# Optimization experiments

Hardware: AMD Instinct MI355X
Metric: run time of the kernel (lower is better)

## Reference

```python
import jax, jax.numpy as jnp
import numpy as np

D_K = 64  # per-head dim, hardcoded in the original module


def setup_inputs() -> dict:
    key = jax.random.key(0)
    kq, kk, kv, km = jax.random.split(key, 4)
    B, H, S, D = 4, 16, 2048, 64
    Q = jax.random.normal(kq, (B, H, S, D), dtype=jnp.float32)
    K = jax.random.normal(kk, (B, H, S, D), dtype=jnp.float32)
    V = jax.random.normal(kv, (B, H, S, D), dtype=jnp.float32)
    attn_mask = jax.random.randint(km, (B, H, S, S), 0, 2).astype(jnp.bool_)
    return {"Q": Q, "K": K, "V": V, "attn_mask": attn_mask}


def reference(Q, K, V, attn_mask):
    # scores = Q @ K^T / sqrt(d_k)  -> [B, H, S, S]
    scale = 1.0 / np.sqrt(D_K).astype(np.float32)
    scores = jnp.einsum("bhqd,bhkd->bhqk", Q, K) * scale
    scores = jnp.where(attn_mask, jnp.float32(-1e9), scores)
    attn = jax.nn.softmax(scores, axis=-1)
    context = jnp.einsum("bhqk,bhkd->bhqd", attn, V)
    return (context, attn)
```

## Files before the change

### kernel.cpp

```cpp
#include <hip/hip_runtime.h>
#include <stdint.h>

#define S_LEN 2048
#define D_HEAD 64
#define NBH 64
#define QBLK 32
#define KBLK 64
#define NITER (S_LEN / KBLK)

typedef __attribute__((ext_vector_type(8))) short short8;
typedef __attribute__((ext_vector_type(4))) float f32x4;

#define KB_OFF   0
#define VT_OFF   24576
#define PRED_OFF 40960
#define P_OFF    49152
#define LP_OFF   53248
#define SMEM_BYTES 53504

#define FK_OFF  0
#define FVT_OFF 16384
#define FP_OFF  24576
#define FMB_OFF 28672
#define FLP_OFF 36864
#define FSMEM_BYTES 37120

__device__ __forceinline__ int swz1(int row, int b) {
  return row * 128 + (b ^ ((row & 7) << 4));
}
__device__ __forceinline__ int swz2(int row, int b) {
  return row * 128 + (b ^ (((row >> 1) & 7) << 4));
}

__device__ __forceinline__ short f2b(float x) {
  unsigned u = __float_as_uint(x);
  unsigned r = 0x7FFFu + ((u >> 16) & 1u);
  return (short)((u + r) >> 16);
}
__device__ __forceinline__ float b2f(short s) {
  return __uint_as_float(((unsigned)(unsigned short)s) << 16);
}

__device__ __forceinline__ void gload_lds16(const void* g, void* l) {
  __builtin_amdgcn_global_load_lds(
      (const __attribute__((address_space(1))) unsigned int*)g,
      (__attribute__((address_space(3))) unsigned int*)l, 16, 0, 0);
}

#define WAITBAR(N) do { \
  asm volatile("s_waitcnt vmcnt(" #N ") lgkmcnt(0)" ::: "memory"); \
  __builtin_amdgcn_s_barrier(); } while (0)

__global__ void detect_mask_kernel(const unsigned* m, int* flag) {
  unsigned v = m[blockIdx.x * 256 + threadIdx.x];
  if (v != 0u && v != 1u && v != 0x3F800000u) atomicOr(flag, 1);
}

__global__ void __launch_bounds__(256) convK_kernel(
    const float* __restrict__ in, short* __restrict__ out) {
  size_t i = ((size_t)blockIdx.x * 256 + threadIdx.x) * 8;
  float4 a = ((const float4*)(in + i))[0];
  float4 b = ((const float4*)(in + i))[1];
  short8 v;
  v[0] = f2b(a.x); v[1] = f2b(a.y); v[2] = f2b(a.z); v[3] = f2b(a.w);
  v[4] = f2b(b.x); v[5] = f2b(b.y); v[6] = f2b(b.z); v[7] = f2b(b.w);
  *(short8*)(out + i) = v;
}

__global__ void __launch_bounds__(256) convVT_kernel(
    const float* __restrict__ V, short* __restrict__ out) {
  __shared__ __align__(16) short t[64 * 72];
  int tid = threadIdx.x;
  int kb = blockIdx.x * 64, bh = blockIdx.y;
  const float* src = V + ((size_t)bh * S_LEN + kb) * D_HEAD;
#pragma unroll
  for (int j = 0; j < 4; ++j) {
    int key = j * 16 + (tid >> 4), d0 = (tid & 15) * 4;
    float4 f = *(const float4*)(src + (size_t)key * D_HEAD + d0);
    t[(d0 + 0) * 72 + key] = f2b(f.x);
    t[(d0 + 1) * 72 + key] = f2b(f.y);
    t[(d0 + 2) * 72 + key] = f2b(f.z);
    t[(d0 + 3) * 72 + key] = f2b(f.w);
  }
  __syncthreads();
  int row = tid >> 2, seg = tid & 3;
  short8 v0 = *(const short8*)(t + row * 72 + seg * 16);
  short8 v1 = *(const short8*)(t + row * 72 + seg * 16 + 8);
  short* dst = out + (size_t)bh * D_HEAD * S_LEN + (size_t)row * S_LEN + kb + seg * 16;
  *(short8*)dst = v0;
  *(short8*)(dst + 8) = v1;
}

template <bool BYTEMASK>
__device__ __forceinline__ void attn_fast(
    char* smem, const float* Qg, const void* maskg,
    const short* Kbf, const short* Vtb, float* ctxg, float* attng,
    int qb, int bh) {

  const int tid = threadIdx.x;
  const int w = tid >> 6, l = tid & 63;
  const int lg = l >> 4, li = l & 15;
  const int rh = w >> 1, ch = w & 1;
  const int qbase = qb * QBLK;
  const int row = tid >> 3, seg = tid & 7;

  const float* Qp = Qg + ((size_t)bh * S_LEN + qbase) * D_HEAD;
  const short* Kbp = Kbf + (size_t)bh * S_LEN * D_HEAD;
  const short* Vtp = Vtb + (size_t)bh * D_HEAD * S_LEN;
  float* attnp = attng + ((size_t)bh * S_LEN + qbase) * S_LEN;
  float* ctxp  = ctxg  + ((size_t)bh * S_LEN + qbase) * D_HEAD;
  const size_t mbase = ((size_t)bh * S_LEN + qbase + row) * S_LEN + seg * 8;

  auto stageK = [&](int it) {
    const int buf = it % 3;
    const int r0 = w * 16 + (l >> 3), ci = l & 7;
#pragma unroll
    for (int j = 0; j < 2; ++j) {
      int r = r0 + j * 8;
      const short* src = Kbp + ((size_t)(it * KBLK + r)) * D_HEAD + ((ci ^ (r & 7)) * 8);
      int off = __builtin_amdgcn_readfirstlane(buf * 8192 + (w * 16 + j * 8) * 128);
      gload_lds16(src, smem + KB_OFF + off);
    }
  };
  auto stageVt = [&](int it) {
    const int buf = it & 1;
    const int d0 = w * 16 + (l >> 3), ci = l & 7;
#pragma unroll
    for (int j = 0; j < 2; ++j) {
      int d = d0 + j * 8;
      const short* src = Vtp + (size_t)d * S_LEN + it * KBLK + ((ci ^ (d & 7)) * 8);
      int off = __builtin_amdgcn_readfirstlane(buf * 8192 + (w * 16 + j * 8) * 128);
      gload_lds16(src, smem + VT_OFF + off);
    }
  };

  auto qkt = [&](f32x4* accs, const short8* qf, int it) {
    char* kb = smem + KB_OFF + (it % 3) * 8192;
#pragma unroll
    for (int ct = 0; ct < 2; ++ct) {
      int key = ch * 32 + ct * 16 + li;
      short8 b0 = *(const short8*)(kb + swz1(key, lg * 16));
      short8 b1 = *(const short8*)(kb + swz1(key, 64 + lg * 16));
      accs[ct] = __builtin_amdgcn_mfma_f32_16x16x32_bf16(qf[0], b0, accs[ct], 0, 0, 0);
      accs[ct] = __builtin_amdgcn_mfma_f32_16x16x32_bf16(qf[1], b1, accs[ct], 0, 0, 0);
    }
  };

  struct MaskRegs { int4 a, b; uint2 c; };
  auto loadMask = [&](int it, MaskRegs& m) {
    if constexpr (BYTEMASK) {
      m.c = *(const uint2*)((const unsigned char*)maskg + mbase + it * KBLK);
    } else {
      const int* p = (const int*)maskg + mbase + it * KBLK;
      m.a = *(const int4*)p;
      m.b = *(const int4*)(p + 4);
    }
  };
  auto predWrite = [&](int it, const MaskRegs& m) {
    unsigned pb = 0;
    if constexpr (BYTEMASK) {
      unsigned lo = m.c.x, hi = m.c.y;
#pragma unroll
      for (int j = 0; j < 4; ++j) {
        pb |= (((lo >> (8 * j)) & 255u) != 0u ? 1u : 0u) << j;
        pb |= (((hi >> (8 * j)) & 255u) != 0u ? 1u : 0u) << (j + 4);
      }
    } else {
      pb |= (m.a.x != 0) ? 1u : 0u;
      pb |= (m.a.y != 0) ? 2u : 0u;
      pb |= (m.a.z != 0) ? 4u : 0u;
      pb |= (m.a.w != 0) ? 8u : 0u;
      pb |= (m.b.x != 0) ? 16u : 0u;
      pb |= (m.b.y != 0) ? 32u : 0u;
      pb |= (m.b.z != 0) ? 64u : 0u;
      pb |= (m.b.w != 0) ? 128u : 0u;
    }
    *(unsigned char*)(smem + PRED_OFF + it * 256 + row * 8 + seg) = (unsigned char)pb;
  };

  MaskRegs t0, t1, mA, mB;
  loadMask(0, t0); loadMask(1, t1); loadMask(2, mA); loadMask(3, mB);
  stageK(0); stageK(1);
  {
    const float* src = Qp + row * D_HEAD + seg * 8;
    float4 a = ((const float4*)src)[0];
    float4 b = ((const float4*)src)[1];
    short8 v;
    v[0] = f2b(a.x); v[1] = f2b(a.y); v[2] = f2b(a.z); v[3] = f2b(a.w);
    v[4] = f2b(b.x); v[5] = f2b(b.y); v[6] = f2b(b.z); v[7] = f2b(b.w);
    *(short8*)(smem + P_OFF + swz1(row, seg * 16)) = v;
  }
  __syncthreads();
  short8 qfrag[2];
  {
    int qr = rh * 16 + li;
    qfrag[0] = *(const short8*)(smem + P_OFF + swz1(qr, lg * 16));
    qfrag[1] = *(const short8*)(smem + P_OFF + swz1(qr, 64 + lg * 16));
  }
  predWrite(0, t0);
  predWrite(1, t1);

  float l_acc[4] = {0.f, 0.f, 0.f, 0.f};

  auto p1iter = [&](int i, MaskRegs& m) {
    f32x4 accs[2] = {{0.f,0.f,0.f,0.f},{0.f,0.f,0.f,0.f}};
    qkt(accs, qfrag, i);
    if (i <= 27) {
      if constexpr (BYTEMASK) WAITBAR(1); else WAITBAR(2);
    } else {
      WAITBAR(0);
    }
    if (i + 2 < NITER) stageK(i + 2);
    if (i + 2 < NITER) predWrite(i + 2, m);
    if (i + 4 < NITER) loadMask(i + 4, m);
#pragma unroll
    for (int reg = 0; reg < 4; ++reg) {
      int rw = rh * 16 + lg * 4 + reg;
      unsigned long long p64 =
          *(const unsigned long long*)(smem + PRED_OFF + i * 256 + rw * 8);
      unsigned pw = (unsigned)(p64 >> (ch << 5));
      float e0 = ((pw >> li) & 1u)        ? 0.f : __expf(accs[0][reg] * 0.125f);
      float e1 = ((pw >> (16 + li)) & 1u) ? 0.f : __expf(accs[1][reg] * 0.125f);
      float s = e0 + e1;
      s += __shfl_xor(s, 1);
      s += __shfl_xor(s, 2);
      s += __shfl_xor(s, 4);
      s += __shfl_xor(s, 8);
      l_acc[reg] += s;
    }
  };

  for (int i = 0; i < NITER; i += 2) {
    p1iter(i, mA);
    p1iter(i + 1, mB);
  }

  if (li == 0) {
#pragma unroll
    for (int reg = 0; reg < 4; ++reg)
      *(float*)(smem + LP_OFF + ch * 128 + (rh * 16 + lg * 4 + reg) * 4) = l_acc[reg];
  }
  stageK(0); stageK(1); stageVt(0);
  WAITBAR(4);
  float linv[4];
#pragma unroll
  for (int reg = 0; reg < 4; ++reg) {
    int rw = rh * 16 + lg * 4 + reg;
    linv[reg] = 1.0f / (*(const float*)(smem + LP_OFF + rw * 4) +
                        *(const float*)(smem + LP_OFF + 128 + rw * 4));
  }
  float* attnrow[4];
#pragma unroll
  for (int reg = 0; reg < 4; ++reg)
    attnrow[reg] = attnp + (size_t)(rh * 16 + lg * 4 + reg) * S_LEN + ch * 32 + li;

  f32x4 acco[2] = {{0.f,0.f,0.f,0.f},{0.f,0.f,0.f,0.f}};
  for (int i = 0; i < NITER; ++i) {
    f32x4 accs[2] = {{0.f,0.f,0.f,0.f},{0.f,0.f,0.f,0.f}};
    qkt(accs, qfrag, i);
    asm volatile("s_waitcnt lgkmcnt(0)" ::: "memory");
    __builtin_amdgcn_s_barrier();
    if (i + 2 < NITER) stageK(i + 2);
    if (i + 1 < NITER) stageVt(i + 1);
#pragma unroll
    for (int reg = 0; reg < 4; ++reg) {
      int rw = rh * 16 + lg * 4 + reg;
      unsigned long long p64 =
          *(const unsigned long long*)(smem + PRED_OFF + i * 256 + rw * 8);
      unsigned pw = (unsigned)(p64 >> (ch << 5));
      float e0 = ((pw >> li) & 1u)        ? 0.f : __expf(accs[0][reg] * 0.125f) * linv[reg];
      float e1 = ((pw >> (16 + li)) & 1u) ? 0.f : __expf(accs[1][reg] * 0.125f) * linv[reg];
      attnrow[reg][i * KBLK] = e0;
      attnrow[reg][i * KBLK + 16] = e1;
      *(short*)(smem + P_OFF + swz2(rw, (ch * 32 + li) * 2)) = f2b(e0);
      *(short*)(smem + P_OFF + swz2(rw, (ch * 32 + 16 + li) * 2)) = f2b(e1);
    }
    if (i == 0) WAITBAR(12);
    else if (i <= 29) WAITBAR(20);
    else WAITBAR(8);
    {
      char* vb = smem + VT_OFF + (i & 1) * 8192;
#pragma unroll
      for (int ks = 0; ks < 2; ++ks) {
        int prow = rh * 16 + li;
        short8 af = *(const short8*)(smem + P_OFF + swz2(prow, ks * 64 + lg * 16));
#pragma unroll
        for (int ct2 = 0; ct2 < 2; ++ct2) {
          int d = ch * 32 + ct2 * 16 + li;
          short8 bf = *(const short8*)(vb + swz1(d, ks * 64 + lg * 16));
          acco[ct2] = __builtin_amdgcn_mfma_f32_16x16x32_bf16(af, bf, acco[ct2], 0, 0, 0);
        }
      }
    }
  }

#pragma unroll
  for (int ct2 = 0; ct2 < 2; ++ct2)
#pragma unroll
    for (int reg = 0; reg < 4; ++reg) {
      int rw = rh * 16 + lg * 4 + reg;
      int d = ch * 32 + ct2 * 16 + li;
      ctxp[(size_t)rw * D_HEAD + d] = acco[ct2][reg];
    }
}

__global__ void __launch_bounds__(256, 3)
attn_fast_kernel(const float* Q, const void* M, const short* Kbf, const short* Vtb,
                 float* ctx, float* attn, const int* flag) {
  extern __shared__ char smem[];
  int bid = blockIdx.x;
  int s = ((bid & 7) << 9) | (bid >> 3);
  int bh = s >> 6, qb = s & 63;
  if (*flag)
    attn_fast<true>(smem, Q, M, Kbf, Vtb, ctx, attn, qb, bh);
  else
    attn_fast<false>(smem, Q, M, Kbf, Vtb, ctx, attn, qb, bh);
}

template <bool BYTEMASK>
__device__ __forceinline__ void attn_body(
    char* smem, const float* Qg, const float* Kg, const float* Vg,
    const void* maskg, float* ctxg, float* attng) {

  const int tid = threadIdx.x;
  const int w = tid >> 6, l = tid & 63;
  const int lg = l >> 4, li = l & 15;
  const int rh = w >> 1, ch = w & 1;
  const int qb = blockIdx.x, bh = blockIdx.y;
  const int qbase = qb * QBLK;

  const float* Qp = Qg + ((size_t)bh * S_LEN + qbase) * D_HEAD;
  const float* Kp = Kg + (size_t)bh * S_LEN * D_HEAD;
  const float* Vp = Vg + (size_t)bh * S_LEN * D_HEAD;
  float* attnp = attng + ((size_t)bh * S_LEN + qbase) * S_LEN;
  float* ctxp  = ctxg  + ((size_t)bh * S_LEN + qbase) * D_HEAD;
  const size_t mrow0 = ((size_t)bh * S_LEN + qbase) * S_LEN;

  auto stageK = [&](int it, int buf) {
    char* kb = smem + FK_OFF + buf * 8192;
    int key = tid >> 2, seg = tid & 3;
    const float* src = Kp + ((size_t)(it * KBLK + key)) * D_HEAD + seg * 16;
    float4 f0 = ((const float4*)src)[0];
    float4 f1 = ((const float4*)src)[1];
    float4 f2 = ((const float4*)src)[2];
    float4 f3 = ((const float4*)src)[3];
    short8 v0, v1;
    v0[0] = f2b(f0.x); v0[1] = f2b(f0.y); v0[2] = f2b(f0.z); v0[3] = f2b(f0.w);
    v0[4] = f2b(f1.x); v0[5] = f2b(f1.y); v0[6] = f2b(f1.z); v0[7] = f2b(f1.w);
    v1[0] = f2b(f2.x); v1[1] = f2b(f2.y); v1[2] = f2b(f2.z); v1[3] = f2b(f2.w);
    v1[4] = f2b(f3.x); v1[5] = f2b(f3.y); v1[6] = f2b(f3.z); v1[7] = f2b(f3.w);
    *(short8*)(kb + swz1(key, seg * 32)) = v0;
    *(short8*)(kb + swz1(key, seg * 32 + 16)) = v1;
  };

  auto stageVt = [&](int it) {
    char* vb = smem + FVT_OFF;
    int key = l, db = w;
    const float* src = Vp + ((size_t)(it * KBLK + key)) * D_HEAD + db * 16;
#pragma unroll
    for (int j = 0; j < 4; ++j) {
      float4 f = ((const float4*)src)[j];
      int dd = db * 16 + j * 4;
      *(short*)(vb + swz1(dd + 0, key * 2)) = f2b(f.x);
      *(short*)(vb + swz1(dd + 1, key * 2)) = f2b(f.y);
      *(short*)(vb + swz1(dd + 2, key * 2)) = f2b(f.z);
      *(short*)(vb + swz1(dd + 3, key * 2)) = f2b(f.w);
    }
  };

  auto loadMask = [&](int it, unsigned* m) {
#pragma unroll
    for (int reg = 0; reg < 4; ++reg) {
      int rw = rh * 16 + lg * 4 + reg;
#pragma unroll
      for (int ct = 0; ct < 2; ++ct) {
        size_t idx = mrow0 + (size_t)rw * S_LEN + it * KBLK + ch * 32 + ct * 16 + li;
        if constexpr (BYTEMASK)
          m[ct * 4 + reg] = (unsigned)((const unsigned char*)maskg)[idx];
        else
          m[ct * 4 + reg] = ((const unsigned*)maskg)[idx];
      }
    }
  };

  auto qkt = [&](f32x4* accs, const short8* qf, int buf) {
    char* kb = smem + FK_OFF + buf * 8192;
#pragma unroll
    for (int ct = 0; ct < 2; ++ct) {
      int key = ch * 32 + ct * 16 + li;
      short8 b0 = *(const short8*)(kb + swz1(key, lg * 16));
      short8 b1 = *(const short8*)(kb + swz1(key, 64 + lg * 16));
      accs[ct] = __builtin_amdgcn_mfma_f32_16x16x32_bf16(qf[0], b0, accs[ct], 0, 0, 0);
      accs[ct] = __builtin_amdgcn_mfma_f32_16x16x32_bf16(qf[1], b1, accs[ct], 0, 0, 0);
    }
  };

  stageK(0, 0);
  unsigned mc[8];
  loadMask(0, mc);
  {
    int rw = tid >> 3, seg = tid & 7;
    const float* src = Qp + rw * D_HEAD + seg * 8;
    float4 a = ((const float4*)src)[0];
    float4 b = ((const float4*)src)[1];
    short8 v;
    v[0] = f2b(a.x); v[1] = f2b(a.y); v[2] = f2b(a.z); v[3] = f2b(a.w);
    v[4] = f2b(b.x); v[5] = f2b(b.y); v[6] = f2b(b.z); v[7] = f2b(b.w);
    *(short8*)(smem + FP_OFF + swz1(rw, seg * 16)) = v;
  }
  __syncthreads();
  short8 qfrag[2];
  {
    int rw = rh * 16 + li;
    qfrag[0] = *(const short8*)(smem + FP_OFF + swz1(rw, lg * 16));
    qfrag[1] = *(const short8*)(smem + FP_OFF + swz1(rw, 64 + lg * 16));
  }
  __syncthreads();

  float l_acc[4] = {0.f, 0.f, 0.f, 0.f};
  for (int it = 0; it < NITER; ++it) {
    const int cb = it & 1, nb = cb ^ 1;
    if (it + 1 < NITER) stageK(it + 1, nb);
    unsigned mn[8];
    if (it + 1 < NITER) loadMask(it + 1, mn);
    f32x4 accs[2] = {{0.f,0.f,0.f,0.f},{0.f,0.f,0.f,0.f}};
    qkt(accs, qfrag, cb);
    unsigned mbyte = 0;
#pragma unroll
    for (int reg = 0; reg < 4; ++reg) {
      float contrib = 0.f;
#pragma unroll
      for (int ct = 0; ct < 2; ++ct) {
        bool pred = mc[ct * 4 + reg] != 0u;
        mbyte |= (unsigned)pred << (ct * 4 + reg);
        float p = pred ? 0.f : __expf(accs[ct][reg] * 0.125f);
        contrib += p;
      }
      contrib += __shfl_xor(contrib, 1);
      contrib += __shfl_xor(contrib, 2);
      contrib += __shfl_xor(contrib, 4);
      contrib += __shfl_xor(contrib, 8);
      l_acc[reg] += contrib;
    }
    *(unsigned char*)(smem + FMB_OFF + it * 256 + tid) = (unsigned char)mbyte;
    __syncthreads();
    if (it + 1 < NITER) {
#pragma unroll
      for (int i = 0; i < 8; ++i) mc[i] = mn[i];
    }
  }

  if (li == 0) {
#pragma unroll
    for (int reg = 0; reg < 4; ++reg)
      *(float*)(smem + FLP_OFF + ch * 128 + (rh * 16 + lg * 4 + reg) * 4) = l_acc[reg];
  }
  stageK(0, 0);
  stageVt(0);
  __syncthreads();
  float linv[4];
#pragma unroll
  for (int reg = 0; reg < 4; ++reg) {
    int rw = rh * 16 + lg * 4 + reg;
    linv[reg] = 1.0f / (*(const float*)(smem + FLP_OFF + rw * 4) +
                        *(const float*)(smem + FLP_OFF + 128 + rw * 4));
  }

  f32x4 acco[2] = {{0.f,0.f,0.f,0.f},{0.f,0.f,0.f,0.f}};
  for (int it = 0; it < NITER; ++it) {
    const int cb = it & 1, nb = cb ^ 1;
    if (it > 0) stageVt(it);
    if (it + 1 < NITER) stageK(it + 1, nb);
    f32x4 accs[2] = {{0.f,0.f,0.f,0.f},{0.f,0.f,0.f,0.f}};
    qkt(accs, qfrag, cb);
    unsigned mbyte = *(const unsigned char*)(smem + FMB_OFF + it * 256 + tid);
#pragma unroll
    for (int reg = 0; reg < 4; ++reg) {
      int rw = rh * 16 + lg * 4 + reg;
#pragma unroll
      for (int ct = 0; ct < 2; ++ct) {
        int col = ch * 32 + ct * 16 + li;
        bool pred = (mbyte >> (ct * 4 + reg)) & 1u;
        float p = pred ? 0.f : __expf(accs[ct][reg] * 0.125f) * linv[reg];
        attnp[(size_t)rw * S_LEN + it * KBLK + col] = p;
        *(short*)(smem + FP_OFF + swz2(rw, col * 2)) = f2b(p);
      }
    }
    __syncthreads();
#pragma unroll
    for (int ks = 0; ks < 2; ++ks) {
      int prow = rh * 16 + li;
      short8 af = *(const short8*)(smem + FP_OFF + swz2(prow, ks * 64 + lg * 16));
#pragma unroll
      for (int ct2 = 0; ct2 < 2; ++ct2) {
        int d = ch * 32 + ct2 * 16 + li;
        short8 bf = *(const short8*)(smem + FVT_OFF + swz1(d, ks * 64 + lg * 16));
        acco[ct2] = __builtin_amdgcn_mfma_f32_16x16x32_bf16(af, bf, acco[ct2], 0, 0, 0);
      }
    }
    __syncthreads();
  }

#pragma unroll
  for (int ct2 = 0; ct2 < 2; ++ct2) {
#pragma unroll
    for (int reg = 0; reg < 4; ++reg) {
      int rw = rh * 16 + lg * 4 + reg;
      int d = ch * 32 + ct2 * 16 + li;
      ctxp[(size_t)rw * D_HEAD + d] = acco[ct2][reg];
    }
  }
}

__global__ void __launch_bounds__(256, 4)
attn_kernel(const float* Q, const float* K, const float* V, const void* M,
            float* ctx, float* attn, const int* flag) {
  extern __shared__ char smem[];
  if (*flag)
    attn_body<true>(smem, Q, K, V, M, ctx, attn);
  else
    attn_body<false>(smem, Q, K, V, M, ctx, attn);
}

extern "C" void kernel_launch(void* const* d_in, const int* in_sizes, int n_in,
                              void* d_out, int out_size, void* d_ws, size_t ws_size,
                              hipStream_t stream) {
  const float* Q = (const float*)d_in[0];
  const float* K = (const float*)d_in[1];
  const float* V = (const float*)d_in[2];
  const void*  M = d_in[3];
  float* ctx  = (float*)d_out;
  float* attn = ctx + (size_t)NBH * S_LEN * D_HEAD;
  int* flag = (int*)d_ws;
  short* Kbf = (short*)((char*)d_ws + 256);
  short* Vtb = Kbf + (size_t)NBH * S_LEN * D_HEAD;
  const size_t PRE_BYTES = 256 + (size_t)2 * NBH * S_LEN * D_HEAD * sizeof(short);

  hipMemsetAsync(flag, 0, sizeof(int), stream);
  detect_mask_kernel<<<dim3(16), dim3(256), 0, stream>>>((const unsigned*)M, flag);

  if (ws_size >= PRE_BYTES) {
    convK_kernel<<<dim3(4096), dim3(256), 0, stream>>>(K, Kbf);
    convVT_kernel<<<dim3(32, 64), dim3(256), 0, stream>>>(V, Vtb);
    attn_fast_kernel<<<dim3(4096), dim3(256), SMEM_BYTES, stream>>>(
        Q, M, Kbf, Vtb, ctx, attn, flag);
  } else {
    dim3 grid(S_LEN / QBLK, NBH);
    attn_kernel<<<grid, dim3(256), FSMEM_BYTES, stream>>>(
        Q, K, V, M, ctx, attn, flag);
  }
}
```

Before: 634.5 us.

## Cache unnormalized bf16 probabilities in registers to skip second QK^T pass

Pass 1 now stores the exp'd scores, packed as bf16 pairs, in a fully unrolled per-thread register array (32x4 words). Pass 2 reuses these instead of restaging K and recomputing QK^T and exp, and normalization moves to a scale on the output. Q is prescaled by log2(e)/sqrt(d) so exp2f replaces __expf. The cost is much higher register pressure (launch bounds lowered to 2 blocks per SM) and attention probabilities written at bf16 precision instead of fp32, which may hurt accuracy.

Result: slower. 1.239 ms (+95.3%).

```diff
diff --git a/kernel.cpp b/kernel.cpp
--- a/kernel.cpp
+++ b/kernel.cpp
@@ -1,4 +1,5 @@
 #include <hip/hip_runtime.h>
+#include <hip/hip_bf16.h>
 #include <stdint.h>
 
 #define S_LEN 2048
@@ -8,6 +9,8 @@
 #define KBLK 64
 #define NITER (S_LEN / KBLK)
 
+#define QSCALE 0.1803368801111244f
+
 typedef __attribute__((ext_vector_type(8))) short short8;
 typedef __attribute__((ext_vector_type(4))) float f32x4;
 
@@ -39,6 +42,11 @@
 }
 __device__ __forceinline__ float b2f(short s) {
   return __uint_as_float(((unsigned)(unsigned short)s) << 16);
+}
+__device__ __forceinline__ unsigned pack2bf(float e0, float e1) {
+  union { __hip_bfloat162 h; unsigned u; } cv;
+  cv.h = __float22bfloat162_rn(float2{e0, e1});
+  return cv.u;
 }
 
 __device__ __forceinline__ void gload_lds16(const void* g, void* l) {
@@ -186,8 +194,10 @@
     float4 a = ((const float4*)src)[0];
     float4 b = ((const float4*)src)[1];
     short8 v;
-    v[0] = f2b(a.x); v[1] = f2b(a.y); v[2] = f2b(a.z); v[3] = f2b(a.w);
-    v[4] = f2b(b.x); v[5] = f2b(b.y); v[6] = f2b(b.z); v[7] = f2b(b.w);
+    v[0] = f2b(a.x * QSCALE); v[1] = f2b(a.y * QSCALE);
+    v[2] = f2b(a.z * QSCALE); v[3] = f2b(a.w * QSCALE);
+    v[4] = f2b(b.x * QSCALE); v[5] = f2b(b.y * QSCALE);
+    v[6] = f2b(b.z * QSCALE); v[7] = f2b(b.w * QSCALE);
     *(short8*)(smem + P_OFF + swz1(row, seg * 16)) = v;
   }
   __syncthreads();
@@ -200,9 +210,11 @@
   predWrite(0, t0);
   predWrite(1, t1);
 
+  unsigned p[NITER][4];
   float l_acc[4] = {0.f, 0.f, 0.f, 0.f};
 
-  auto p1iter = [&](int i, MaskRegs& m) {
+#pragma unroll
+  for (int i = 0; i < NITER; ++i) {
     f32x4 accs[2] = {{0.f,0.f,0.f,0.f},{0.f,0.f,0.f,0.f}};
     qkt(accs, qfrag, i);
     if (i <= 27) {
@@ -211,16 +223,17 @@
       WAITBAR(0);
     }
     if (i + 2 < NITER) stageK(i + 2);
-    if (i + 2 < NITER) predWrite(i + 2, m);
-    if (i + 4 < NITER) loadMask(i + 4, m);
+    if (i + 2 < NITER) predWrite(i + 2, (i & 1) ? mB : mA);
+    if (i + 4 < NITER) loadMask(i + 4, (i & 1) ? mB : mA);
 #pragma unroll
     for (int reg = 0; reg < 4; ++reg) {
       int rw = rh * 16 + lg * 4 + reg;
       unsigned long long p64 =
           *(const unsigned long long*)(smem + PRED_OFF + i * 256 + rw * 8);
       unsigned pw = (unsigned)(p64 >> (ch << 5));
-      float e0 = ((pw >> li) & 1u)        ? 0.f : __expf(accs[0][reg] * 0.125f);
-      float e1 = ((pw >> (16 + li)) & 1u) ? 0.f : __expf(accs[1][reg] * 0.125f);
+      float e0 = ((pw >> li) & 1u)        ? 0.f : exp2f(accs[0][reg]);
+      float e1 = ((pw >> (16 + li)) & 1u) ? 0.f : exp2f(accs[1][reg]);
+      p[i][reg] = pack2bf(e0, e1);
       float s = e0 + e1;
       s += __shfl_xor(s, 1);
       s += __shfl_xor(s, 2);
@@ -228,11 +241,6 @@
       s += __shfl_xor(s, 8);
       l_acc[reg] += s;
     }
-  };
-
-  for (int i = 0; i < NITER; i += 2) {
-    p1iter(i, mA);
-    p1iter(i + 1, mB);
   }
 
   if (li == 0) {
@@ -240,8 +248,8 @@
     for (int reg = 0; reg < 4; ++reg)
       *(float*)(smem + LP_OFF + ch * 128 + (rh * 16 + lg * 4 + reg) * 4) = l_acc[reg];
   }
-  stageK(0); stageK(1); stageVt(0);
-  WAITBAR(4);
+  stageVt(0);
+  WAITBAR(0);
   float linv[4];
 #pragma unroll
   for (int reg = 0; reg < 4; ++reg) {
@@ -255,29 +263,27 @@
     attnrow[reg] = attnp + (size_t)(rh * 16 + lg * 4 + reg) * S_LEN + ch * 32 + li;
 
   f32x4 acco[2] = {{0.f,0.f,0.f,0.f},{0.f,0.f,0.f,0.f}};
+#pragma unroll
   for (int i = 0; i < NITER; ++i) {
-    f32x4 accs[2] = {{0.f,0.f,0.f,0.f},{0.f,0.f,0.f,0.f}};
-    qkt(accs, qfrag, i);
+#pragma unroll
+    for (int reg = 0; reg < 4; ++reg) {
+      unsigned pu = p[i][reg];
+      float e0 = __uint_as_float(pu << 16) * linv[reg];
+      float e1 = __uint_as_float(pu & 0xffff0000u) * linv[reg];
+      attnrow[reg][i * KBLK] = e0;
+      attnrow[reg][i * KBLK + 16] = e1;
+    }
     asm volatile("s_waitcnt lgkmcnt(0)" ::: "memory");
     __builtin_amdgcn_s_barrier();
-    if (i + 2 < NITER) stageK(i + 2);
+#pragma unroll
+    for (int reg = 0; reg < 4; ++reg) {
+      int rw = rh * 16 + lg * 4 + reg;
+      unsigned pu = p[i][reg];
+      *(short*)(smem + P_OFF + swz2(rw, (ch * 32 + li) * 2)) = (short)(pu & 0xffffu);
+      *(short*)(smem + P_OFF + swz2(rw, (ch * 32 + 16 + li) * 2)) = (short)(pu >> 16);
+    }
     if (i + 1 < NITER) stageVt(i + 1);
-#pragma unroll
-    for (int reg = 0; reg < 4; ++reg) {
-      int rw = rh * 16 + lg * 4 + reg;
-      unsigned long long p64 =
-          *(const unsigned long long*)(smem + PRED_OFF + i * 256 + rw * 8);
-      unsigned pw = (unsigned)(p64 >> (ch << 5));
-      float e0 = ((pw >> li) & 1u)        ? 0.f : __expf(accs[0][reg] * 0.125f) * linv[reg];
-      float e1 = ((pw >> (16 + li)) & 1u) ? 0.f : __expf(accs[1][reg] * 0.125f) * linv[reg];
-      attnrow[reg][i * KBLK] = e0;
-      attnrow[reg][i * KBLK + 16] = e1;
-      *(short*)(smem + P_OFF + swz2(rw, (ch * 32 + li) * 2)) = f2b(e0);
-      *(short*)(smem + P_OFF + swz2(rw, (ch * 32 + 16 + li) * 2)) = f2b(e1);
-    }
-    if (i == 0) WAITBAR(12);
-    else if (i <= 29) WAITBAR(20);
-    else WAITBAR(8);
+    if (i + 1 < NITER) { WAITBAR(10); } else { WAITBAR(8); }
     {
       char* vb = smem + VT_OFF + (i & 1) * 8192;
 #pragma unroll
@@ -300,11 +306,11 @@
     for (int reg = 0; reg < 4; ++reg) {
       int rw = rh * 16 + lg * 4 + reg;
       int d = ch * 32 + ct2 * 16 + li;
-      ctxp[(size_t)rw * D_HEAD + d] = acco[ct2][reg];
-    }
-}
-
-__global__ void __launch_bounds__(256, 3)
+      ctxp[(size_t)rw * D_HEAD + d] = acco[ct2][reg] * linv[reg];
+    }
+}
+
+__global__ void __launch_bounds__(256, 2)
 attn_fast_kernel(const float* Q, const void* M, const short* Kbf, const short* Vtb,
                  float* ctx, float* attn, const int* flag) {
   extern __shared__ char smem[];
@@ -433,8 +439,8 @@
       for (int ct = 0; ct < 2; ++ct) {
         bool pred = mc[ct * 4 + reg] != 0u;
         mbyte |= (unsigned)pred << (ct * 4 + reg);
-        float p = pred ? 0.f : __expf(accs[ct][reg] * 0.125f);
-        contrib += p;
+        float pp = pred ? 0.f : __expf(accs[ct][reg] * 0.125f);
+        contrib += pp;
       }
       contrib += __shfl_xor(contrib, 1);
       contrib += __shfl_xor(contrib, 2);
@@ -481,9 +487,9 @@
       for (int ct = 0; ct < 2; ++ct) {
         int col = ch * 32 + ct * 16 + li;
         bool pred = (mbyte >> (ct * 4 + reg)) & 1u;
-        float p = pred ? 0.f : __expf(accs[ct][reg] * 0.125f) * linv[reg];
-        attnp[(size_t)rw * S_LEN + it * KBLK + col] = p;
-        *(short*)(smem + FP_OFF + swz2(rw, col * 2)) = f2b(p);
+        float pp = pred ? 0.f : __expf(accs[ct][reg] * 0.125f) * linv[reg];
+        attnp[(size_t)rw * S_LEN + it * KBLK + col] = pp;
+        *(short*)(smem + FP_OFF + swz2(rw, col * 2)) = f2b(pp);
       }
     }
     __syncthreads();
```

## Split fused attention into separate row-sum and output passes via global predicate buffer

Applied to the files above, without the earlier changes.

The single fused kernel is split into two launches. The first pass computes softmax row sums and packed mask bits, storing the bits in the context output buffer as scratch and the reciprocal sums in workspace. The second pass reloads them, recomputes QK^T, and writes attn and ctx. The aim is higher occupancy for the first pass (4 blocks per CU) and less per-kernel shared memory. Folding log2(e)/sqrt(d) into Q so exp2f replaces the expf-with-scale is a separate small change. The cost is an extra launch and a round trip of predicate data through global memory.

Result: slower. 697.9 us (+10.0%).

```diff
diff --git a/kernel.cpp b/kernel.cpp
--- a/kernel.cpp
+++ b/kernel.cpp
@@ -1,4 +1,5 @@
 #include <hip/hip_runtime.h>
+#include <hip/hip_bf16.h>
 #include <stdint.h>
 
 #define S_LEN 2048
@@ -8,15 +9,22 @@
 #define KBLK 64
 #define NITER (S_LEN / KBLK)
 
+#define QSCALE 0.1803368801111244f
+
 typedef __attribute__((ext_vector_type(8))) short short8;
 typedef __attribute__((ext_vector_type(4))) float f32x4;
 
-#define KB_OFF   0
-#define VT_OFF   24576
-#define PRED_OFF 40960
-#define P_OFF    49152
-#define LP_OFF   53248
-#define SMEM_BYTES 53504
+#define AKB   0
+#define APRED 24576
+#define AP    32768
+#define ALP   36864
+#define ASMEM 37120
+
+#define BKB   0
+#define BVT   24576
+#define BPRED 40960
+#define BP    49152
+#define BSMEM 53248
 
 #define FK_OFF  0
 #define FVT_OFF 16384
@@ -36,9 +44,6 @@
   unsigned u = __float_as_uint(x);
   unsigned r = 0x7FFFu + ((u >> 16) & 1u);
   return (short)((u + r) >> 16);
-}
-__device__ __forceinline__ float b2f(short s) {
-  return __uint_as_float(((unsigned)(unsigned short)s) << 16);
 }
 
 __device__ __forceinline__ void gload_lds16(const void* g, void* l) {
@@ -92,10 +97,9 @@
 }
 
 template <bool BYTEMASK>
-__device__ __forceinline__ void attn_fast(
-    char* smem, const float* Qg, const void* maskg,
-    const short* Kbf, const short* Vtb, float* ctxg, float* attng,
-    int qb, int bh) {
+__device__ __forceinline__ void pass1_body(
+    char* smem, const float* Qg, const void* maskg, const short* Kbf,
+    unsigned char* predg, float* linvg, int qb, int bh, int sidx) {
 
   const int tid = threadIdx.x;
   const int w = tid >> 6, l = tid & 63;
@@ -106,9 +110,6 @@
 
   const float* Qp = Qg + ((size_t)bh * S_LEN + qbase) * D_HEAD;
   const short* Kbp = Kbf + (size_t)bh * S_LEN * D_HEAD;
-  const short* Vtp = Vtb + (size_t)bh * D_HEAD * S_LEN;
-  float* attnp = attng + ((size_t)bh * S_LEN + qbase) * S_LEN;
-  float* ctxp  = ctxg  + ((size_t)bh * S_LEN + qbase) * D_HEAD;
   const size_t mbase = ((size_t)bh * S_LEN + qbase + row) * S_LEN + seg * 8;
 
   auto stageK = [&](int it) {
@@ -119,23 +120,11 @@
       int r = r0 + j * 8;
       const short* src = Kbp + ((size_t)(it * KBLK + r)) * D_HEAD + ((ci ^ (r & 7)) * 8);
       int off = __builtin_amdgcn_readfirstlane(buf * 8192 + (w * 16 + j * 8) * 128);
-      gload_lds16(src, smem + KB_OFF + off);
-    }
-  };
-  auto stageVt = [&](int it) {
-    const int buf = it & 1;
-    const int d0 = w * 16 + (l >> 3), ci = l & 7;
-#pragma unroll
-    for (int j = 0; j < 2; ++j) {
-      int d = d0 + j * 8;
-      const short* src = Vtp + (size_t)d * S_LEN + it * KBLK + ((ci ^ (d & 7)) * 8);
-      int off = __builtin_amdgcn_readfirstlane(buf * 8192 + (w * 16 + j * 8) * 128);
-      gload_lds16(src, smem + VT_OFF + off);
-    }
-  };
-
+      gload_lds16(src, smem + AKB + off);
+    }
+  };
   auto qkt = [&](f32x4* accs, const short8* qf, int it) {
-    char* kb = smem + KB_OFF + (it % 3) * 8192;
+    char* kb = smem + AKB + (it % 3) * 8192;
 #pragma unroll
     for (int ct = 0; ct < 2; ++ct) {
       int key = ch * 32 + ct * 16 + li;
@@ -175,7 +164,7 @@
       pb |= (m.b.z != 0) ? 64u : 0u;
       pb |= (m.b.w != 0) ? 128u : 0u;
     }
-    *(unsigned char*)(smem + PRED_OFF + it * 256 + row * 8 + seg) = (unsigned char)pb;
+    *(unsigned char*)(smem + APRED + it * 256 + row * 8 + seg) = (unsigned char)pb;
   };
 
   MaskRegs t0, t1, mA, mB;
@@ -186,22 +175,23 @@
     float4 a = ((const float4*)src)[0];
     float4 b = ((const float4*)src)[1];
     short8 v;
-    v[0] = f2b(a.x); v[1] = f2b(a.y); v[2] = f2b(a.z); v[3] = f2b(a.w);
-    v[4] = f2b(b.x); v[5] = f2b(b.y); v[6] = f2b(b.z); v[7] = f2b(b.w);
-    *(short8*)(smem + P_OFF + swz1(row, seg * 16)) = v;
+    v[0] = f2b(a.x * QSCALE); v[1] = f2b(a.y * QSCALE);
+    v[2] = f2b(a.z * QSCALE); v[3] = f2b(a.w * QSCALE);
+    v[4] = f2b(b.x * QSCALE); v[5] = f2b(b.y * QSCALE);
+    v[6] = f2b(b.z * QSCALE); v[7] = f2b(b.w * QSCALE);
+    *(short8*)(smem + AP + swz1(row, seg * 16)) = v;
   }
   __syncthreads();
   short8 qfrag[2];
   {
     int qr = rh * 16 + li;
-    qfrag[0] = *(const short8*)(smem + P_OFF + swz1(qr, lg * 16));
-    qfrag[1] = *(const short8*)(smem + P_OFF + swz1(qr, 64 + lg * 16));
+    qfrag[0] = *(const short8*)(smem + AP + swz1(qr, lg * 16));
+    qfrag[1] = *(const short8*)(smem + AP + swz1(qr, 64 + lg * 16));
   }
   predWrite(0, t0);
   predWrite(1, t1);
 
   float l_acc[4] = {0.f, 0.f, 0.f, 0.f};
-
   auto p1iter = [&](int i, MaskRegs& m) {
     f32x4 accs[2] = {{0.f,0.f,0.f,0.f},{0.f,0.f,0.f,0.f}};
     qkt(accs, qfrag, i);
@@ -217,10 +207,10 @@
     for (int reg = 0; reg < 4; ++reg) {
       int rw = rh * 16 + lg * 4 + reg;
       unsigned long long p64 =
-          *(const unsigned long long*)(smem + PRED_OFF + i * 256 + rw * 8);
+          *(const unsigned long long*)(smem + APRED + i * 256 + rw * 8);
       unsigned pw = (unsigned)(p64 >> (ch << 5));
-      float e0 = ((pw >> li) & 1u)        ? 0.f : __expf(accs[0][reg] * 0.125f);
-      float e1 = ((pw >> (16 + li)) & 1u) ? 0.f : __expf(accs[1][reg] * 0.125f);
+      float e0 = ((pw >> li) & 1u)        ? 0.f : exp2f(accs[0][reg]);
+      float e1 = ((pw >> (16 + li)) & 1u) ? 0.f : exp2f(accs[1][reg]);
       float s = e0 + e1;
       s += __shfl_xor(s, 1);
       s += __shfl_xor(s, 2);
@@ -229,7 +219,6 @@
       l_acc[reg] += s;
     }
   };
-
   for (int i = 0; i < NITER; i += 2) {
     p1iter(i, mA);
     p1iter(i + 1, mB);
@@ -238,21 +227,126 @@
   if (li == 0) {
 #pragma unroll
     for (int reg = 0; reg < 4; ++reg)
-      *(float*)(smem + LP_OFF + ch * 128 + (rh * 16 + lg * 4 + reg) * 4) = l_acc[reg];
-  }
-  stageK(0); stageK(1); stageVt(0);
-  WAITBAR(4);
+      *(float*)(smem + ALP + ch * 128 + (rh * 16 + lg * 4 + reg) * 4) = l_acc[reg];
+  }
+  __syncthreads();
+  if (ch == 0 && li == 0) {
+#pragma unroll
+    for (int reg = 0; reg < 4; ++reg) {
+      int rw = rh * 16 + lg * 4 + reg;
+      float tot = *(const float*)(smem + ALP + rw * 4) +
+                  *(const float*)(smem + ALP + 128 + rw * 4);
+      linvg[(size_t)bh * S_LEN + qbase + rw] = 1.0f / tot;
+    }
+  }
+  unsigned char* pd = predg + (size_t)sidx * 8192;
+  *(uint4*)(pd + tid * 16) = *(const uint4*)(smem + APRED + tid * 16);
+  *(uint4*)(pd + 4096 + tid * 16) = *(const uint4*)(smem + APRED + 4096 + tid * 16);
+}
+
+__global__ void __launch_bounds__(256, 4)
+attn_pass1_kernel(const float* Q, const void* M, const short* Kbf,
+                  unsigned char* predg, float* linvg, const int* flag) {
+  __shared__ __align__(16) char smem[ASMEM];
+  int bid = blockIdx.x;
+  int s = ((bid & 7) << 9) | (bid >> 3);
+  int bh = s >> 6, qb = s & 63;
+  if (*flag)
+    pass1_body<true>(smem, Q, M, Kbf, predg, linvg, qb, bh, s);
+  else
+    pass1_body<false>(smem, Q, M, Kbf, predg, linvg, qb, bh, s);
+}
+
+__global__ void __launch_bounds__(256, 3)
+attn_pass2_kernel(const float* Qg, const short* Kbf, const short* Vtb,
+                  const unsigned char* predg, const float* linvg,
+                  float* ctxg, float* attng) {
+  __shared__ __align__(16) char smem[BSMEM];
+  const int tid = threadIdx.x;
+  const int w = tid >> 6, l = tid & 63;
+  const int lg = l >> 4, li = l & 15;
+  const int rh = w >> 1, ch = w & 1;
+  int bid = blockIdx.x;
+  int s = ((bid & 7) << 9) | (bid >> 3);
+  int bh = s >> 6, qb = s & 63;
+  const int qbase = qb * QBLK;
+  const int row = tid >> 3, seg = tid & 7;
+
+  const float* Qp = Qg + ((size_t)bh * S_LEN + qbase) * D_HEAD;
+  const short* Kbp = Kbf + (size_t)bh * S_LEN * D_HEAD;
+  const short* Vtp = Vtb + (size_t)bh * D_HEAD * S_LEN;
+  float* attnp = attng + ((size_t)bh * S_LEN + qbase) * S_LEN;
+  float* ctxp  = ctxg  + ((size_t)bh * S_LEN + qbase) * D_HEAD;
+
+  auto stageK = [&](int it) {
+    const int buf = it % 3;
+    const int r0 = w * 16 + (l >> 3), ci = l & 7;
+#pragma unroll
+    for (int j = 0; j < 2; ++j) {
+      int r = r0 + j * 8;
+      const short* src = Kbp + ((size_t)(it * KBLK + r)) * D_HEAD + ((ci ^ (r & 7)) * 8);
+      int off = __builtin_amdgcn_readfirstlane(buf * 8192 + (w * 16 + j * 8) * 128);
+      gload_lds16(src, smem + BKB + off);
+    }
+  };
+  auto stageVt = [&](int it) {
+    const int buf = it & 1;
+    const int d0 = w * 16 + (l >> 3), ci = l & 7;
+#pragma unroll
+    for (int j = 0; j < 2; ++j) {
+      int d = d0 + j * 8;
+      const short* src = Vtp + (size_t)d * S_LEN + it * KBLK + ((ci ^ (d & 7)) * 8);
+      int off = __builtin_amdgcn_readfirstlane(buf * 8192 + (w * 16 + j * 8) * 128);
+      gload_lds16(src, smem + BVT + off);
+    }
+  };
+  auto qkt = [&](f32x4* accs, const short8* qf, int it) {
+    char* kb = smem + BKB + (it % 3) * 8192;
+#pragma unroll
+    for (int ct = 0; ct < 2; ++ct) {
+      int key = ch * 32 + ct * 16 + li;
+      short8 b0 = *(const short8*)(kb + swz1(key, lg * 16));
+      short8 b1 = *(const short8*)(kb + swz1(key, 64 + lg * 16));
+      accs[ct] = __builtin_amdgcn_mfma_f32_16x16x32_bf16(qf[0], b0, accs[ct], 0, 0, 0);
+      accs[ct] = __builtin_amdgcn_mfma_f32_16x16x32_bf16(qf[1], b1, accs[ct], 0, 0, 0);
+    }
+  };
+
+  stageK(0); stageK(1);
+  const unsigned char* pd = predg + (size_t)s * 8192;
+  uint4 pg0 = *(const uint4*)(pd + tid * 16);
+  uint4 pg1 = *(const uint4*)(pd + 4096 + tid * 16);
+  {
+    const float* src = Qp + row * D_HEAD + seg * 8;
+    float4 a = ((const float4*)src)[0];
+    float4 b = ((const float4*)src)[1];
+    short8 v;
+    v[0] = f2b(a.x * QSCALE); v[1] = f2b(a.y * QSCALE);
+    v[2] = f2b(a.z * QSCALE); v[3] = f2b(a.w * QSCALE);
+    v[4] = f2b(b.x * QSCALE); v[5] = f2b(b.y * QSCALE);
+    v[6] = f2b(b.z * QSCALE); v[7] = f2b(b.w * QSCALE);
+    *(short8*)(smem + BP + swz1(row, seg * 16)) = v;
+  }
+  __syncthreads();
+  short8 qfrag[2];
+  {
+    int qr = rh * 16 + li;
+    qfrag[0] = *(const short8*)(smem + BP + swz1(qr, lg * 16));
+    qfrag[1] = *(const short8*)(smem + BP + swz1(qr, 64 + lg * 16));
+  }
+  *(uint4*)(smem + BPRED + tid * 16) = pg0;
+  *(uint4*)(smem + BPRED + 4096 + tid * 16) = pg1;
   float linv[4];
 #pragma unroll
-  for (int reg = 0; reg < 4; ++reg) {
-    int rw = rh * 16 + lg * 4 + reg;
-    linv[reg] = 1.0f / (*(const float*)(smem + LP_OFF + rw * 4) +
-                        *(const float*)(smem + LP_OFF + 128 + rw * 4));
-  }
+  for (int reg = 0; reg < 4; ++reg)
+    linv[reg] = linvg[(size_t)bh * S_LEN + qbase + rh * 16 + lg * 4 + reg];
   float* attnrow[4];
 #pragma unroll
   for (int reg = 0; reg < 4; ++reg)
     attnrow[reg] = attnp + (size_t)(rh * 16 + lg * 4 + reg) * S_LEN + ch * 32 + li;
+  stageVt(0);
+  asm volatile("s_waitcnt lgkmcnt(0)" ::: "memory");
+  __builtin_amdgcn_s_barrier();
 
   f32x4 acco[2] = {{0.f,0.f,0.f,0.f},{0.f,0.f,0.f,0.f}};
   for (int i = 0; i < NITER; ++i) {
@@ -266,24 +360,24 @@
     for (int reg = 0; reg < 4; ++reg) {
       int rw = rh * 16 + lg * 4 + reg;
       unsigned long long p64 =
-          *(const unsigned long long*)(smem + PRED_OFF + i * 256 + rw * 8);
+          *(const unsigned long long*)(smem + BPRED + i * 256 + rw * 8);
       unsigned pw = (unsigned)(p64 >> (ch << 5));
-      float e0 = ((pw >> li) & 1u)        ? 0.f : __expf(accs[0][reg] * 0.125f) * linv[reg];
-      float e1 = ((pw >> (16 + li)) & 1u) ? 0.f : __expf(accs[1][reg] * 0.125f) * linv[reg];
+      float e0 = ((pw >> li) & 1u)        ? 0.f : exp2f(accs[0][reg]) * linv[reg];
+      float e1 = ((pw >> (16 + li)) & 1u) ? 0.f : exp2f(accs[1][reg]) * linv[reg];
       attnrow[reg][i * KBLK] = e0;
       attnrow[reg][i * KBLK + 16] = e1;
-      *(short*)(smem + P_OFF + swz2(rw, (ch * 32 + li) * 2)) = f2b(e0);
-      *(short*)(smem + P_OFF + swz2(rw, (ch * 32 + 16 + li) * 2)) = f2b(e1);
+      *(short*)(smem + BP + swz2(rw, (ch * 32 + li) * 2)) = f2b(e0);
+      *(short*)(smem + BP + swz2(rw, (ch * 32 + 16 + li) * 2)) = f2b(e1);
     }
     if (i == 0) WAITBAR(12);
     else if (i <= 29) WAITBAR(20);
     else WAITBAR(8);
     {
-      char* vb = smem + VT_OFF + (i & 1) * 8192;
+      char* vb = smem + BVT + (i & 1) * 8192;
 #pragma unroll
       for (int ks = 0; ks < 2; ++ks) {
         int prow = rh * 16 + li;
-        short8 af = *(const short8*)(smem + P_OFF + swz2(prow, ks * 64 + lg * 16));
+        short8 af = *(const short8*)(smem + BP + swz2(prow, ks * 64 + lg * 16));
 #pragma unroll
         for (int ct2 = 0; ct2 < 2; ++ct2) {
           int d = ch * 32 + ct2 * 16 + li;
@@ -304,19 +398,6 @@
     }
 }
 
-__global__ void __launch_bounds__(256, 3)
-attn_fast_kernel(const float* Q, const void* M, const short* Kbf, const short* Vtb,
-                 float* ctx, float* attn, const int* flag) {
-  extern __shared__ char smem[];
-  int bid = blockIdx.x;
-  int s = ((bid & 7) << 9) | (bid >> 3);
-  int bh = s >> 6, qb = s & 63;
-  if (*flag)
-    attn_fast<true>(smem, Q, M, Kbf, Vtb, ctx, attn, qb, bh);
-  else
-    attn_fast<false>(smem, Q, M, Kbf, Vtb, ctx, attn, qb, bh);
-}
-
 template <bool BYTEMASK>
 __device__ __forceinline__ void attn_body(
     char* smem, const float* Qg, const float* Kg, const float* Vg,
@@ -327,7 +408,7 @@
   const int lg = l >> 4, li = l & 15;
   const int rh = w >> 1, ch = w & 1;
   const int qb = blockIdx.x, bh = blockIdx.y;
-  const int qbase = qb * QBLK;
+  const int qbase = qb * 32;
 
   const float* Qp = Qg + ((size_t)bh * S_LEN + qbase) * D_HEAD;
   const float* Kp = Kg + (size_t)bh * S_LEN * D_HEAD;
@@ -433,8 +514,8 @@
       for (int ct = 0; ct < 2; ++ct) {
         bool pred = mc[ct * 4 + reg] != 0u;
         mbyte |= (unsigned)pred << (ct * 4 + reg);
-        float p = pred ? 0.f : __expf(accs[ct][reg] * 0.125f);
-        contrib += p;
+        float pp = pred ? 0.f : __expf(accs[ct][reg] * 0.125f);
+        contrib += pp;
       }
       contrib += __shfl_xor(contrib, 1);
       contrib += __shfl_xor(contrib, 2);
@@ -481,9 +562,9 @@
       for (int ct = 0; ct < 2; ++ct) {
         int col = ch * 32 + ct * 16 + li;
         bool pred = (mbyte >> (ct * 4 + reg)) & 1u;
-        float p = pred ? 0.f : __expf(accs[ct][reg] * 0.125f) * linv[reg];
-        attnp[(size_t)rw * S_LEN + it * KBLK + col] = p;
-        *(short*)(smem + FP_OFF + swz2(rw, col * 2)) = f2b(p);
+        float pp = pred ? 0.f : __expf(accs[ct][reg] * 0.125f) * linv[reg];
+        attnp[(size_t)rw * S_LEN + it * KBLK + col] = pp;
+        *(short*)(smem + FP_OFF + swz2(rw, col * 2)) = f2b(pp);
       }
     }
     __syncthreads();
@@ -534,7 +615,10 @@
   int* flag = (int*)d_ws;
   short* Kbf = (short*)((char*)d_ws + 256);
   short* Vtb = Kbf + (size_t)NBH * S_LEN * D_HEAD;
-  const size_t PRE_BYTES = 256 + (size_t)2 * NBH * S_LEN * D_HEAD * sizeof(short);
+  float* linvg = (float*)(Vtb + (size_t)NBH * S_LEN * D_HEAD);
+  unsigned char* predg = (unsigned char*)ctx;
+  const size_t PRE_BYTES = 256 + (size_t)2 * NBH * S_LEN * D_HEAD * sizeof(short)
+                         + (size_t)NBH * S_LEN * sizeof(float);
 
   hipMemsetAsync(flag, 0, sizeof(int), stream);
   detect_mask_kernel<<<dim3(16), dim3(256), 0, stream>>>((const unsigned*)M, flag);
@@ -542,10 +626,12 @@
   if (ws_size >= PRE_BYTES) {
     convK_kernel<<<dim3(4096), dim3(256), 0, stream>>>(K, Kbf);
     convVT_kernel<<<dim3(32, 64), dim3(256), 0, stream>>>(V, Vtb);
-    attn_fast_kernel<<<dim3(4096), dim3(256), SMEM_BYTES, stream>>>(
-        Q, M, Kbf, Vtb, ctx, attn, flag);
+    attn_pass1_kernel<<<dim3(4096), dim3(256), 0, stream>>>(
+        Q, M, Kbf, predg, linvg, flag);
+    attn_pass2_kernel<<<dim3(4096), dim3(256), 0, stream>>>(
+        Q, Kbf, Vtb, predg, linvg, ctx, attn);
   } else {
-    dim3 grid(S_LEN / QBLK, NBH);
+    dim3 grid(S_LEN / 32, NBH);
     attn_kernel<<<grid, dim3(256), FSMEM_BYTES, stream>>>(
         Q, K, V, M, ctx, attn, flag);
   }
```

## Coalesce attention-matrix stores via LDS readback and fold softmax scale into Q

Applied to the files above, without the earlier changes.

The attention matrix is now written back as contiguous 16-byte vectors per thread. These are read from the bf16 P tile already staged in LDS, replacing the earlier scattered 4-byte stores from the MFMA layout. The 1/sqrt(d)·log2(e) factor is folded into Q during bf16 conversion, so exp2f is used directly. The row-sum shuffle reduction moves out of the first-pass loop, and the vmcnt wait thresholds are retuned to the smaller store count. The stored attention probabilities are now bf16-rounded rather than full fp32, which adds numerical error to that output.

Result: slower. 651.3 us (+2.6%).

```diff
diff --git a/kernel.cpp b/kernel.cpp
--- a/kernel.cpp
+++ b/kernel.cpp
@@ -1,4 +1,5 @@
 #include <hip/hip_runtime.h>
+#include <hip/hip_bf16.h>
 #include <stdint.h>
 
 #define S_LEN 2048
@@ -8,6 +9,8 @@
 #define KBLK 64
 #define NITER (S_LEN / KBLK)
 
+#define QSCALE 0.1803368801111244f
+
 typedef __attribute__((ext_vector_type(8))) short short8;
 typedef __attribute__((ext_vector_type(4))) float f32x4;
 
@@ -49,6 +52,9 @@
 
 #define WAITBAR(N) do { \
   asm volatile("s_waitcnt vmcnt(" #N ") lgkmcnt(0)" ::: "memory"); \
+  __builtin_amdgcn_s_barrier(); } while (0)
+#define LGKMBAR() do { \
+  asm volatile("s_waitcnt lgkmcnt(0)" ::: "memory"); \
   __builtin_amdgcn_s_barrier(); } while (0)
 
 __global__ void detect_mask_kernel(const unsigned* m, int* flag) {
@@ -93,8 +99,9 @@
 
 template <bool BYTEMASK>
 __device__ __forceinline__ void attn_fast(
-    char* smem, const float* Qg, const void* maskg,
-    const short* Kbf, const short* Vtb, float* ctxg, float* attng,
+    char* smem, const float* __restrict__ Qg, const void* __restrict__ maskg,
+    const short* __restrict__ Kbf, const short* __restrict__ Vtb,
+    float* __restrict__ ctxg, float* __restrict__ attng,
     int qb, int bh) {
 
   const int tid = threadIdx.x;
@@ -186,8 +193,10 @@
     float4 a = ((const float4*)src)[0];
     float4 b = ((const float4*)src)[1];
     short8 v;
-    v[0] = f2b(a.x); v[1] = f2b(a.y); v[2] = f2b(a.z); v[3] = f2b(a.w);
-    v[4] = f2b(b.x); v[5] = f2b(b.y); v[6] = f2b(b.z); v[7] = f2b(b.w);
+    v[0] = f2b(a.x * QSCALE); v[1] = f2b(a.y * QSCALE);
+    v[2] = f2b(a.z * QSCALE); v[3] = f2b(a.w * QSCALE);
+    v[4] = f2b(b.x * QSCALE); v[5] = f2b(b.y * QSCALE);
+    v[6] = f2b(b.z * QSCALE); v[7] = f2b(b.w * QSCALE);
     *(short8*)(smem + P_OFF + swz1(row, seg * 16)) = v;
   }
   __syncthreads();
@@ -201,7 +210,6 @@
   predWrite(1, t1);
 
   float l_acc[4] = {0.f, 0.f, 0.f, 0.f};
-
   auto p1iter = [&](int i, MaskRegs& m) {
     f32x4 accs[2] = {{0.f,0.f,0.f,0.f},{0.f,0.f,0.f,0.f}};
     qkt(accs, qfrag, i);
@@ -219,22 +227,25 @@
       unsigned long long p64 =
           *(const unsigned long long*)(smem + PRED_OFF + i * 256 + rw * 8);
       unsigned pw = (unsigned)(p64 >> (ch << 5));
-      float e0 = ((pw >> li) & 1u)        ? 0.f : __expf(accs[0][reg] * 0.125f);
-      float e1 = ((pw >> (16 + li)) & 1u) ? 0.f : __expf(accs[1][reg] * 0.125f);
-      float s = e0 + e1;
-      s += __shfl_xor(s, 1);
-      s += __shfl_xor(s, 2);
-      s += __shfl_xor(s, 4);
-      s += __shfl_xor(s, 8);
-      l_acc[reg] += s;
-    }
-  };
-
+      float e0 = ((pw >> li) & 1u)        ? 0.f : exp2f(accs[0][reg]);
+      float e1 = ((pw >> (16 + li)) & 1u) ? 0.f : exp2f(accs[1][reg]);
+      l_acc[reg] += e0 + e1;
+    }
+  };
   for (int i = 0; i < NITER; i += 2) {
     p1iter(i, mA);
     p1iter(i + 1, mB);
   }
 
+#pragma unroll
+  for (int reg = 0; reg < 4; ++reg) {
+    float s = l_acc[reg];
+    s += __shfl_xor(s, 1);
+    s += __shfl_xor(s, 2);
+    s += __shfl_xor(s, 4);
+    s += __shfl_xor(s, 8);
+    l_acc[reg] = s;
+  }
   if (li == 0) {
 #pragma unroll
     for (int reg = 0; reg < 4; ++reg)
@@ -249,17 +260,13 @@
     linv[reg] = 1.0f / (*(const float*)(smem + LP_OFF + rw * 4) +
                         *(const float*)(smem + LP_OFF + 128 + rw * 4));
   }
-  float* attnrow[4];
-#pragma unroll
-  for (int reg = 0; reg < 4; ++reg)
-    attnrow[reg] = attnp + (size_t)(rh * 16 + lg * 4 + reg) * S_LEN + ch * 32 + li;
+  float* arow = attnp + (size_t)row * S_LEN + seg * 8;
 
   f32x4 acco[2] = {{0.f,0.f,0.f,0.f},{0.f,0.f,0.f,0.f}};
   for (int i = 0; i < NITER; ++i) {
     f32x4 accs[2] = {{0.f,0.f,0.f,0.f},{0.f,0.f,0.f,0.f}};
     qkt(accs, qfrag, i);
-    asm volatile("s_waitcnt lgkmcnt(0)" ::: "memory");
-    __builtin_amdgcn_s_barrier();
+    LGKMBAR();
     if (i + 2 < NITER) stageK(i + 2);
     if (i + 1 < NITER) stageVt(i + 1);
 #pragma unroll
@@ -268,16 +275,23 @@
       unsigned long long p64 =
           *(const unsigned long long*)(smem + PRED_OFF + i * 256 + rw * 8);
       unsigned pw = (unsigned)(p64 >> (ch << 5));
-      float e0 = ((pw >> li) & 1u)        ? 0.f : __expf(accs[0][reg] * 0.125f) * linv[reg];
-      float e1 = ((pw >> (16 + li)) & 1u) ? 0.f : __expf(accs[1][reg] * 0.125f) * linv[reg];
-      attnrow[reg][i * KBLK] = e0;
-      attnrow[reg][i * KBLK + 16] = e1;
+      float e0 = ((pw >> li) & 1u)        ? 0.f : exp2f(accs[0][reg]) * linv[reg];
+      float e1 = ((pw >> (16 + li)) & 1u) ? 0.f : exp2f(accs[1][reg]) * linv[reg];
       *(short*)(smem + P_OFF + swz2(rw, (ch * 32 + li) * 2)) = f2b(e0);
       *(short*)(smem + P_OFF + swz2(rw, (ch * 32 + 16 + li) * 2)) = f2b(e1);
     }
-    if (i == 0) WAITBAR(12);
-    else if (i <= 29) WAITBAR(20);
-    else WAITBAR(8);
+    if (i == 0) WAITBAR(4);
+    else if (i <= 29) WAITBAR(6);
+    else if (i == 30) WAITBAR(4);
+    else WAITBAR(2);
+    {
+      short8 pv = *(const short8*)(smem + P_OFF + swz2(row, seg * 16));
+      float4 f0, f1;
+      f0.x = b2f(pv[0]); f0.y = b2f(pv[1]); f0.z = b2f(pv[2]); f0.w = b2f(pv[3]);
+      f1.x = b2f(pv[4]); f1.y = b2f(pv[5]); f1.z = b2f(pv[6]); f1.w = b2f(pv[7]);
+      ((float4*)(arow + i * KBLK))[0] = f0;
+      *(float4*)(arow + i * KBLK + 4) = f1;
+    }
     {
       char* vb = smem + VT_OFF + (i & 1) * 8192;
 #pragma unroll
@@ -307,7 +321,7 @@
 __global__ void __launch_bounds__(256, 3)
 attn_fast_kernel(const float* Q, const void* M, const short* Kbf, const short* Vtb,
                  float* ctx, float* attn, const int* flag) {
-  extern __shared__ char smem[];
+  __shared__ __align__(16) char smem[SMEM_BYTES];
   int bid = blockIdx.x;
   int s = ((bid & 7) << 9) | (bid >> 3);
   int bh = s >> 6, qb = s & 63;
@@ -327,7 +341,7 @@
   const int lg = l >> 4, li = l & 15;
   const int rh = w >> 1, ch = w & 1;
   const int qb = blockIdx.x, bh = blockIdx.y;
-  const int qbase = qb * QBLK;
+  const int qbase = qb * 32;
 
   const float* Qp = Qg + ((size_t)bh * S_LEN + qbase) * D_HEAD;
   const float* Kp = Kg + (size_t)bh * S_LEN * D_HEAD;
@@ -433,8 +447,8 @@
       for (int ct = 0; ct < 2; ++ct) {
         bool pred = mc[ct * 4 + reg] != 0u;
         mbyte |= (unsigned)pred << (ct * 4 + reg);
-        float p = pred ? 0.f : __expf(accs[ct][reg] * 0.125f);
-        contrib += p;
+        float pp = pred ? 0.f : __expf(accs[ct][reg] * 0.125f);
+        contrib += pp;
       }
       contrib += __shfl_xor(contrib, 1);
       contrib += __shfl_xor(contrib, 2);
@@ -481,9 +495,9 @@
       for (int ct = 0; ct < 2; ++ct) {
         int col = ch * 32 + ct * 16 + li;
         bool pred = (mbyte >> (ct * 4 + reg)) & 1u;
-        float p = pred ? 0.f : __expf(accs[ct][reg] * 0.125f) * linv[reg];
-        attnp[(size_t)rw * S_LEN + it * KBLK + col] = p;
-        *(short*)(smem + FP_OFF + swz2(rw, col * 2)) = f2b(p);
+        float pp = pred ? 0.f : __expf(accs[ct][reg] * 0.125f) * linv[reg];
+        attnp[(size_t)rw * S_LEN + it * KBLK + col] = pp;
+        *(short*)(smem + FP_OFF + swz2(rw, col * 2)) = f2b(pp);
       }
     }
     __syncthreads();
@@ -542,10 +556,10 @@
   if (ws_size >= PRE_BYTES) {
     convK_kernel<<<dim3(4096), dim3(256), 0, stream>>>(K, Kbf);
     convVT_kernel<<<dim3(32, 64), dim3(256), 0, stream>>>(V, Vtb);
-    attn_fast_kernel<<<dim3(4096), dim3(256), SMEM_BYTES, stream>>>(
+    attn_fast_kernel<<<dim3(4096), dim3(256), 0, stream>>>(
         Q, M, Kbf, Vtb, ctx, attn, flag);
   } else {
-    dim3 grid(S_LEN / QBLK, NBH);
+    dim3 grid(S_LEN / 32, NBH);
     attn_kernel<<<grid, dim3(256), FSMEM_BYTES, stream>>>(
         Q, K, V, M, ctx, attn, flag);
   }
```
